# Optimization experiments

Hardware: AMD Instinct MI355X
Metric: run time of the kernel (lower is better)

Reference implementation:

```python
import jax, jax.numpy as jnp
import numpy as np

B, N, K, E, H, V = 128, 256, 4, 300, 150, 32000  # batch, nodes/tree, max children, embed, hidden, vocab
DELTA = 1.0


def setup_inputs() -> dict:
    key = jax.random.key(0)
    ks = jax.random.split(key, 8)
    query = jax.random.randint(ks[0], (B, N), 0, V, dtype=jnp.int32)
    pos = jax.random.randint(ks[1], (B, N), 0, V, dtype=jnp.int32)
    neg = jax.random.randint(ks[2], (B, N), 0, V, dtype=jnp.int32)
    # Complete K-ary tree over N nodes: children of node t are {K*t+1, ..., K*t+K} < N; root = node 0.
    ch = np.full((N, K), -1, dtype=np.int32)
    for t in range(N):
        for j in range(K):
            c = K * t + 1 + j
            if c < N:
                ch[t, j] = c
    children = jnp.asarray(ch)
    emb = jax.random.normal(ks[3], (V, E), dtype=jnp.float32) * 0.02
    W_iou = jax.random.normal(ks[4], (E, 3 * H), dtype=jnp.float32) * 0.05
    U_iou = jax.random.normal(ks[5], (H, 3 * H), dtype=jnp.float32) * 0.05
    b_iou = jnp.zeros((3 * H,), jnp.float32)
    W_f = jax.random.normal(ks[6], (E, H), dtype=jnp.float32) * 0.05
    U_f = jax.random.normal(ks[7], (H, H), dtype=jnp.float32) * 0.05
    b_f = jnp.zeros((H,), jnp.float32)
    return {"query": query, "pos": pos, "neg": neg, "children": children,
            "emb": emb, "W_iou": W_iou, "U_iou": U_iou, "b_iou": b_iou,
            "W_f": W_f, "U_f": U_f, "b_f": b_f}


def _childsum_treelstm(x, children, W_iou, U_iou, b_iou, W_f, U_f, b_f):
    """x: [B, N, E] node embeddings. Returns root (c, h): each [B, H]."""
    Bn, Nn, _ = x.shape
    Hh = U_f.shape[0]
    h0 = jnp.zeros((Bn, Nn, Hh), x.dtype)
    c0 = jnp.zeros((Bn, Nn, Hh), x.dtype)

    def step(carry, t):
        h_all, c_all = carry
        ch = children[t]                        # [K] child indices, -1 = padding
        mask = (ch >= 0)
        idx = jnp.where(mask, ch, 0)
        m = mask.astype(x.dtype)[None, :, None]  # [1, K, 1]
        h_k = h_all[:, idx] * m                 # [B, K, H]
        c_k = c_all[:, idx] * m
        h_sum = h_k.sum(axis=1)                 # child-sum h_tilde [B, H]
        x_t = x[:, t]                           # [B, E]
        iou = x_t @ W_iou + h_sum @ U_iou + b_iou
        i, o, u = jnp.split(iou, 3, axis=-1)
        i = jax.nn.sigmoid(i)
        o = jax.nn.sigmoid(o)
        u = jnp.tanh(u)
        # per-child forget gates: f_jk = sigmoid(W_f x_j + U_f h_k + b_f)
        f = jax.nn.sigmoid((x_t @ W_f + b_f)[:, None, :] + h_k @ U_f)  # [B, K, H]
        c_t = i * u + (f * c_k).sum(axis=1)     # c_k already masked
        h_t = o * jnp.tanh(c_t)
        return (h_all.at[:, t].set(h_t), c_all.at[:, t].set(c_t)), None

    # children have larger indices than parents -> process N-1 .. 0 (root last)
    (h_all, c_all), _ = jax.lax.scan(step, (h0, c0), jnp.arange(Nn - 1, -1, -1))
    return c_all[:, 0], h_all[:, 0]


def _cosine(a, b):
    num = (a * b).sum(-1)
    den = jnp.sqrt((a * a).sum(-1) * (b * b).sum(-1)) + 1e-8
    return num / den


def reference(query, pos, neg, children, emb, W_iou, U_iou, b_iou, W_f, U_f, b_f):
    qc, _ = _childsum_treelstm(emb[query], children, W_iou, U_iou, b_iou, W_f, U_f, b_f)
    pc, _ = _childsum_treelstm(emb[pos], children, W_iou, U_iou, b_iou, W_f, U_f, b_f)
    nc, _ = _childsum_treelstm(emb[neg], children, W_iou, U_iou, b_iou, W_f, U_f, b_f)
    a = _cosine(qc, pc)  # [B]
    b = _cosine(qc, nc)  # [B]
    return jax.nn.relu(DELTA - a + b)
```

## Files before the change

kernel.cpp:

```cpp
#include <hip/hip_runtime.h>
#include <hip/hip_bf16.h>

typedef short short8 __attribute__((ext_vector_type(8)));
typedef float floatx4 __attribute__((ext_vector_type(4)));
typedef unsigned short ushort;

#define Bb 128
#define Nn 256
#define Hh 150
#define HK 160
#define Vv 32000
#define NROW 384
#define PROJC 640
#define NINT 64
#define ZROW (Vv + NROW * NINT)

__device__ __forceinline__ float sigf(float x) { return 1.0f / (1.0f + __expf(-x)); }
__device__ __forceinline__ float tanhf_(float x) { return 1.0f - 2.0f / (__expf(2.0f * x) + 1.0f); }
__device__ __forceinline__ float bf2f(ushort s) { union { float f; unsigned u; } v; v.u = ((unsigned)s) << 16; return v.f; }
__device__ __forceinline__ ushort f2bf(float f) { __hip_bfloat16 h = __float2bfloat16(f); return *(ushort*)&h; }

__global__ __launch_bounds__(256) void k_prep(
    const float* __restrict__ W_iou, const float* __restrict__ W_f,
    const float* __restrict__ U_iou, const float* __restrict__ U_f,
    const float* __restrict__ b_iou, const float* __restrict__ b_f,
    short* __restrict__ Wt, short* __restrict__ Uti, short* __restrict__ Utf,
    float* __restrict__ biasw, ushort* __restrict__ h_u, float* __restrict__ c_u)
{
    int idx = blockIdx.x * 256 + threadIdx.x;
    const int nWt = PROJC * 320, nUi = 464 * 160, nUf = 160 * 160;
    if (idx < nWt) {
        int n = idx / 320, k = idx % 320;
        int seg = n / 160, cc = n % 160;
        float v = 0.f;
        if (k < 300 && cc < 150) {
            if (seg == 0)      v = W_iou[k * 450 + cc];
            else if (seg == 1) v = W_iou[k * 450 + 150 + cc];
            else if (seg == 2) v = W_iou[k * 450 + 300 + cc];
            else               v = W_f[k * 150 + cc];
        }
        Wt[idx] = (short)f2bf(v);
    } else if (idx < nWt + nUi) {
        int i2 = idx - nWt; int n = i2 / 160, k = i2 % 160;
        float v = (k < 150 && n < 450) ? U_iou[k * 450 + n] : 0.f;
        Uti[i2] = (short)f2bf(v);
    } else if (idx < nWt + nUi + nUf) {
        int i2 = idx - nWt - nUi; int n = i2 / 160, k = i2 % 160;
        float v = (k < 150) ? U_f[k * 150 + n] : 0.f;
        Utf[i2] = (short)f2bf(v);
    } else if (idx < nWt + nUi + nUf + PROJC) {
        int n = idx - nWt - nUi - nUf;
        int seg = n / 160, cc = n % 160;
        biasw[n] = (cc < 150) ? (seg < 3 ? b_iou[seg * 150 + cc] : b_f[cc]) : 0.f;
    } else if (idx < nWt + nUi + nUf + PROJC + HK) {
        int k = idx - (nWt + nUi + nUf + PROJC);
        h_u[(long)ZROW * HK + k] = 0;
        c_u[(long)ZROW * HK + k] = 0.f;
    }
}

__global__ __launch_bounds__(256) void k_vproj(
    const float* __restrict__ emb, const short* __restrict__ Wt,
    const float* __restrict__ biasw, ushort* __restrict__ proj,
    ushort* __restrict__ h_u, float* __restrict__ c_u)
{
    __shared__ __align__(16) short As[32 * 328];
    const int tid = threadIdx.x;
    const int v0 = blockIdx.x * 32;

    for (int i = tid; i < 32 * 80; i += 256) {
        int r = i / 80, q = i % 80, k0 = q * 4;
        short4 sv;
        if (k0 < 300) {
            float4 x = *(const float4*)(emb + (long)(v0 + r) * 300 + k0);
            sv.x = (short)f2bf(x.x); sv.y = (short)f2bf(x.y);
            sv.z = (short)f2bf(x.z); sv.w = (short)f2bf(x.w);
        } else sv = make_short4(0, 0, 0, 0);
        *(short4*)&As[r * 328 + k0] = sv;
    }
    __syncthreads();

    const int w = tid >> 6, lane = tid & 63;
    const int m = lane & 15, kq = (lane >> 4) * 8;

    short8 a0[10], a1[10];
    #pragma unroll
    for (int ks = 0; ks < 10; ks++) {
        a0[ks] = *(const short8*)&As[m * 328 + kq + ks * 32];
        a1[ks] = *(const short8*)&As[(16 + m) * 328 + kq + ks * 32];
    }

    for (int j = w; j < 10; j += 4) {
        int col = j * 16 + m;
        const short* bp = Wt + (long)col * 320 + kq;
        floatx4 acc[4][2];
        #pragma unroll
        for (int s = 0; s < 4; s++) { acc[s][0] = {0.f,0.f,0.f,0.f}; acc[s][1] = {0.f,0.f,0.f,0.f}; }
        #pragma unroll
        for (int ks = 0; ks < 10; ks++) {
            short8 b0 = *(const short8*)(bp + 0 * 160 * 320 + ks * 32);
            short8 b1 = *(const short8*)(bp + 1 * 160 * 320 + ks * 32);
            short8 b2 = *(const short8*)(bp + 2 * 160 * 320 + ks * 32);
            short8 b3 = *(const short8*)(bp + 3 * 160 * 320 + ks * 32);
            acc[0][0] = __builtin_amdgcn_mfma_f32_16x16x32_bf16(a0[ks], b0, acc[0][0], 0, 0, 0);
            acc[0][1] = __builtin_amdgcn_mfma_f32_16x16x32_bf16(a1[ks], b0, acc[0][1], 0, 0, 0);
            acc[1][0] = __builtin_amdgcn_mfma_f32_16x16x32_bf16(a0[ks], b1, acc[1][0], 0, 0, 0);
            acc[1][1] = __builtin_amdgcn_mfma_f32_16x16x32_bf16(a1[ks], b1, acc[1][1], 0, 0, 0);
            acc[2][0] = __builtin_amdgcn_mfma_f32_16x16x32_bf16(a0[ks], b2, acc[2][0], 0, 0, 0);
            acc[2][1] = __builtin_amdgcn_mfma_f32_16x16x32_bf16(a1[ks], b2, acc[2][1], 0, 0, 0);
            acc[3][0] = __builtin_amdgcn_mfma_f32_16x16x32_bf16(a0[ks], b3, acc[3][0], 0, 0, 0);
            acc[3][1] = __builtin_amdgcn_mfma_f32_16x16x32_bf16(a1[ks], b3, acc[3][1], 0, 0, 0);
        }

        float bi_ = biasw[col], bo_ = biasw[160 + col];
        float bu_ = biasw[320 + col], bf_ = biasw[480 + col];
        int rb = (lane >> 4) * 4;
        #pragma unroll
        for (int g = 0; g < 2; g++) {
            #pragma unroll
            for (int reg = 0; reg < 4; reg++) {
                long row = v0 + g * 16 + rb + reg;
                float pi = acc[0][g][reg] + bi_;
                float po = acc[1][g][reg] + bo_;
                float pu = acc[2][g][reg] + bu_;
                float pf = acc[3][g][reg] + bf_;
                ushort* pr = proj + row * PROJC;
                pr[col]       = f2bf(pi);
                pr[160 + col] = f2bf(po);
                pr[320 + col] = f2bf(pu);
                pr[480 + col] = f2bf(pf);
                float iv = sigf(pi), ov = sigf(po), uv = tanhf_(pu);
                float cc = iv * uv;
                c_u[row * HK + col] = cc;
                h_u[row * HK + col] = f2bf(ov * tanhf_(cc));
            }
        }
    }
}

__global__ __launch_bounds__(256) void k_level(
    int t0,
    const int* __restrict__ tq, const int* __restrict__ tp, const int* __restrict__ tn,
    const int* __restrict__ children, const ushort* __restrict__ proj,
    const short* __restrict__ Uti, const short* __restrict__ Utf,
    ushort* __restrict__ h_u, float* __restrict__ c_u)
{
    __shared__ __align__(16) short As[5][16][168];
    __shared__ int idx_s[16][4];
    __shared__ int tok_s[16];

    const int tid = threadIdx.x;
    const int t = t0 + blockIdx.x / 24;
    const int r0 = (blockIdx.x % 24) * 16;

    if (tid < 64) {
        int r = tid >> 2, j = tid & 3;
        int rg = r0 + r, g = rg >> 7, b = rg & 127;
        const int* tok = (g == 0) ? tq : (g == 1 ? tp : tn);
        int ch = children[t * 4 + j];
        int idx;
        if (ch < 0)        idx = ZROW;
        else if (ch >= 64) idx = tok[b * Nn + ch];
        else               idx = Vv + rg * NINT + ch;
        idx_s[r][j] = idx;
        if (j == 0) tok_s[r] = tok[b * Nn + t];
    }
    __syncthreads();

    for (int i = tid; i < 16 * 20; i += 256) {
        int r = i / 20, k0 = (i % 20) * 8;
        int4 v0 = *(const int4*)(h_u + (long)idx_s[r][0] * HK + k0);
        int4 v1 = *(const int4*)(h_u + (long)idx_s[r][1] * HK + k0);
        int4 v2 = *(const int4*)(h_u + (long)idx_s[r][2] * HK + k0);
        int4 v3 = *(const int4*)(h_u + (long)idx_s[r][3] * HK + k0);
        *(int4*)&As[1][r][k0] = v0;
        *(int4*)&As[2][r][k0] = v1;
        *(int4*)&As[3][r][k0] = v2;
        *(int4*)&As[4][r][k0] = v3;
        ushort s[8];
        const ushort* p0 = (const ushort*)&v0; const ushort* p1 = (const ushort*)&v1;
        const ushort* p2 = (const ushort*)&v2; const ushort* p3 = (const ushort*)&v3;
        #pragma unroll
        for (int e = 0; e < 8; e++)
            s[e] = f2bf(bf2f(p0[e]) + bf2f(p1[e]) + bf2f(p2[e]) + bf2f(p3[e]));
        *(int4*)&As[0][r][k0] = *(int4*)s;
    }
    __syncthreads();

    const int w = tid >> 6, lane = tid & 63;
    const int m = lane & 15, kq = (lane >> 4) * 8;
    const int rbase = (lane >> 4) * 4;

    for (int nt = w; nt < 10; nt += 4) {
        int col = nt * 16 + m;

        ushort pg[4][4]; float cg[4][4];
        #pragma unroll
        for (int reg = 0; reg < 4; reg++) {
            const ushort* pr = proj + (long)tok_s[rbase + reg] * PROJC;
            pg[0][reg] = pr[col];
            pg[1][reg] = pr[160 + col];
            pg[2][reg] = pr[320 + col];
            pg[3][reg] = pr[480 + col];
            #pragma unroll
            for (int j = 0; j < 4; j++)
                cg[j][reg] = c_u[(long)idx_s[rbase + reg][j] * HK + col];
        }

        const short* bi  = Uti + (long)(col) * HK + kq;
        const short* bo  = Uti + (long)(150 + col) * HK + kq;
        const short* bu  = Uti + (long)(300 + col) * HK + kq;
        const short* bff = Utf + (long)col * HK + kq;
        floatx4 ai = {0.f,0.f,0.f,0.f}, ao = ai, au = ai;
        floatx4 af0 = ai, af1 = ai, af2 = ai, af3 = ai;
        #pragma unroll
        for (int ks = 0; ks < 5; ks++) {
            short8 asum = *(const short8*)&As[0][m][kq + ks * 32];
            short8 ac0  = *(const short8*)&As[1][m][kq + ks * 32];
            short8 ac1  = *(const short8*)&As[2][m][kq + ks * 32];
            short8 ac2  = *(const short8*)&As[3][m][kq + ks * 32];
            short8 ac3  = *(const short8*)&As[4][m][kq + ks * 32];
            short8 vbi = *(const short8*)(bi + ks * 32);
            short8 vbo = *(const short8*)(bo + ks * 32);
            short8 vbu = *(const short8*)(bu + ks * 32);
            short8 vbf = *(const short8*)(bff + ks * 32);
            ai  = __builtin_amdgcn_mfma_f32_16x16x32_bf16(asum, vbi, ai, 0, 0, 0);
            ao  = __builtin_amdgcn_mfma_f32_16x16x32_bf16(asum, vbo, ao, 0, 0, 0);
            au  = __builtin_amdgcn_mfma_f32_16x16x32_bf16(asum, vbu, au, 0, 0, 0);
            af0 = __builtin_amdgcn_mfma_f32_16x16x32_bf16(ac0,  vbf, af0, 0, 0, 0);
            af1 = __builtin_amdgcn_mfma_f32_16x16x32_bf16(ac1,  vbf, af1, 0, 0, 0);
            af2 = __builtin_amdgcn_mfma_f32_16x16x32_bf16(ac2,  vbf, af2, 0, 0, 0);
            af3 = __builtin_amdgcn_mfma_f32_16x16x32_bf16(ac3,  vbf, af3, 0, 0, 0);
        }

        if (col < Hh) {
            #pragma unroll
            for (int reg = 0; reg < 4; reg++) {
                int rg = r0 + rbase + reg;
                float iv = sigf(bf2f(pg[0][reg])   + ai[reg]);
                float ov = sigf(bf2f(pg[1][reg])   + ao[reg]);
                float uv = tanhf_(bf2f(pg[2][reg]) + au[reg]);
                float fpre = bf2f(pg[3][reg]);
                float cv = iv * uv;
                cv = fmaf(sigf(fpre + af0[reg]), cg[0][reg], cv);
                cv = fmaf(sigf(fpre + af1[reg]), cg[1][reg], cv);
                cv = fmaf(sigf(fpre + af2[reg]), cg[2][reg], cv);
                cv = fmaf(sigf(fpre + af3[reg]), cg[3][reg], cv);
                long o = (long)(Vv + rg * NINT + t) * HK + col;
                c_u[o] = cv;
                h_u[o] = f2bf(ov * tanhf_(cv));
            }
        } else {
            #pragma unroll
            for (int reg = 0; reg < 4; reg++) {
                long o = (long)(Vv + (r0 + rbase + reg) * NINT + t) * HK + col;
                c_u[o] = 0.f; h_u[o] = 0;
            }
        }
    }
}

__global__ __launch_bounds__(64) void k_cos(const float* __restrict__ c_u, float* __restrict__ out)
{
    int b = blockIdx.x, tid = threadIdx.x;
    const float* qc = c_u + (long)(Vv + (0 * Bb + b) * NINT) * HK;
    const float* pc = c_u + (long)(Vv + (1 * Bb + b) * NINT) * HK;
    const float* nc = c_u + (long)(Vv + (2 * Bb + b) * NINT) * HK;
    float qp = 0, qn = 0, qq = 0, pp = 0, nn2 = 0;
    for (int k = tid; k < Hh; k += 64) {
        float qv = qc[k], pv = pc[k], nv = nc[k];
        qp += qv * pv; qn += qv * nv; qq += qv * qv; pp += pv * pv; nn2 += nv * nv;
    }
    #pragma unroll
    for (int off = 32; off > 0; off >>= 1) {
        qp += __shfl_down(qp, off, 64);
        qn += __shfl_down(qn, off, 64);
        qq += __shfl_down(qq, off, 64);
        pp += __shfl_down(pp, off, 64);
        nn2 += __shfl_down(nn2, off, 64);
    }
    if (tid == 0) {
        float a = qp / (sqrtf(qq * pp) + 1e-8f);
        float d = qn / (sqrtf(qq * nn2) + 1e-8f);
        out[b] = fmaxf(0.0f, 1.0f - a + d);
    }
}

extern "C" void kernel_launch(void* const* d_in, const int* in_sizes, int n_in,
                              void* d_out, int out_size, void* d_ws, size_t ws_size,
                              hipStream_t stream)
{
    const int*   tq       = (const int*)d_in[0];
    const int*   tp       = (const int*)d_in[1];
    const int*   tn       = (const int*)d_in[2];
    const int*   children = (const int*)d_in[3];
    const float* emb      = (const float*)d_in[4];
    const float* W_iou    = (const float*)d_in[5];
    const float* U_iou    = (const float*)d_in[6];
    const float* b_iou    = (const float*)d_in[7];
    const float* W_f      = (const float*)d_in[8];
    const float* U_f      = (const float*)d_in[9];
    const float* b_f      = (const float*)d_in[10];
    float* out = (float*)d_out;

    char* ws = (char*)d_ws;
    ushort* proj  = (ushort*)ws;
    ushort* h_u   = (ushort*)(ws + 40960000);
    float*  c_u   = (float*)(ws + 59064640);
    short*  Wt    = (short*)(ws + 95273920);
    short*  Uti   = (short*)(ws + 95683520);
    short*  Utf   = (short*)(ws + 95832000);
    float*  biasw = (float*)(ws + 95883200);

    k_prep<<<1194, 256, 0, stream>>>(W_iou, W_f, U_iou, U_f, b_iou, b_f,
                                     Wt, Uti, Utf, biasw, h_u, c_u);
    k_vproj<<<Vv / 32, 256, 0, stream>>>(emb, Wt, biasw, proj, h_u, c_u);
    k_level<<<43 * 24, 256, 0, stream>>>(21, tq, tp, tn, children, proj, Uti, Utf, h_u, c_u);
    k_level<<<16 * 24, 256, 0, stream>>>(5,  tq, tp, tn, children, proj, Uti, Utf, h_u, c_u);
    k_level<<<4 * 24, 256, 0, stream>>>(1,   tq, tp, tn, children, proj, Uti, Utf, h_u, c_u);
    k_level<<<1 * 24, 256, 0, stream>>>(0,   tq, tp, tn, children, proj, Uti, Utf, h_u, c_u);
    k_cos<<<Bb, 64, 0, stream>>>(c_u, out);
}
```

Before: 286.6 us.

## Store projection in MFMA-fragment layout, coalesce vproj stores, split small levels wider

k_vproj now writes the gate projections in a tiled layout matching the MFMA accumulator fragment, as packed 8-byte stores instead of scattered 2-byte stores. The h/c leaf states are staged through shared memory so they go out as 16-byte row-contiguous writes. k_level computes the matching fragment addresses to read proj, and its small upper levels spread the column tiles over more blocks (G parameter) to raise parallelism. The cost is more complex address arithmetic and gather loads deferred into the epilogue instead of being issued before the MFMA loop.

```diff
diff --git a/kernel.cpp b/kernel.cpp
--- a/kernel.cpp
+++ b/kernel.cpp
@@ -11,7 +11,6 @@
 #define HK 160
 #define Vv 32000
 #define NROW 384
-#define PROJC 640
 #define NINT 64
 #define ZROW (Vv + NROW * NINT)
 
@@ -28,7 +27,7 @@
     float* __restrict__ biasw, ushort* __restrict__ h_u, float* __restrict__ c_u)
 {
     int idx = blockIdx.x * 256 + threadIdx.x;
-    const int nWt = PROJC * 320, nUi = 464 * 160, nUf = 160 * 160;
+    const int nWt = 640 * 320, nUi = 464 * 160, nUf = 160 * 160;
     if (idx < nWt) {
         int n = idx / 320, k = idx % 320;
         int seg = n / 160, cc = n % 160;
@@ -48,12 +47,12 @@
         int i2 = idx - nWt - nUi; int n = i2 / 160, k = i2 % 160;
         float v = (k < 150) ? U_f[k * 150 + n] : 0.f;
         Utf[i2] = (short)f2bf(v);
-    } else if (idx < nWt + nUi + nUf + PROJC) {
+    } else if (idx < nWt + nUi + nUf + 640) {
         int n = idx - nWt - nUi - nUf;
         int seg = n / 160, cc = n % 160;
         biasw[n] = (cc < 150) ? (seg < 3 ? b_iou[seg * 150 + cc] : b_f[cc]) : 0.f;
-    } else if (idx < nWt + nUi + nUf + PROJC + HK) {
-        int k = idx - (nWt + nUi + nUf + PROJC);
+    } else if (idx < nWt + nUi + nUf + 640 + HK) {
+        int k = idx - (nWt + nUi + nUf + 640);
         h_u[(long)ZROW * HK + k] = 0;
         c_u[(long)ZROW * HK + k] = 0.f;
     }
@@ -65,6 +64,8 @@
     ushort* __restrict__ h_u, float* __restrict__ c_u)
 {
     __shared__ __align__(16) short As[32 * 328];
+    __shared__ __align__(16) float Tc[4][32][20];
+    __shared__ __align__(16) ushort Th[4][32][24];
     const int tid = threadIdx.x;
     const int v0 = blockIdx.x * 32;
 
@@ -81,7 +82,7 @@
     __syncthreads();
 
     const int w = tid >> 6, lane = tid & 63;
-    const int m = lane & 15, kq = (lane >> 4) * 8;
+    const int m = lane & 15, quad = lane >> 4, kq = quad * 8;
 
     short8 a0[10], a1[10];
     #pragma unroll
@@ -112,34 +113,55 @@
             acc[3][1] = __builtin_amdgcn_mfma_f32_16x16x32_bf16(a1[ks], b3, acc[3][1], 0, 0, 0);
         }
 
-        float bi_ = biasw[col], bo_ = biasw[160 + col];
-        float bu_ = biasw[320 + col], bf_ = biasw[480 + col];
-        int rb = (lane >> 4) * 4;
-        #pragma unroll
-        for (int g = 0; g < 2; g++) {
+        float bias[4] = { biasw[col], biasw[160 + col], biasw[320 + col], biasw[480 + col] };
+        float pre[4][2][4];
+        #pragma unroll
+        for (int s = 0; s < 4; s++)
+            #pragma unroll
+            for (int g = 0; g < 2; g++)
+                #pragma unroll
+                for (int reg = 0; reg < 4; reg++)
+                    pre[s][g][reg] = acc[s][g][reg] + bias[s];
+
+        long tbase = (long)(blockIdx.x * 10 + j) * 2048;
+        #pragma unroll
+        for (int s = 0; s < 4; s++)
+            #pragma unroll
+            for (int g = 0; g < 2; g++) {
+                unsigned u0 = (unsigned)f2bf(pre[s][g][0]) | ((unsigned)f2bf(pre[s][g][1]) << 16);
+                unsigned u1 = (unsigned)f2bf(pre[s][g][2]) | ((unsigned)f2bf(pre[s][g][3]) << 16);
+                *(uint2*)(proj + tbase + s * 512 + g * 256 + lane * 4) = make_uint2(u0, u1);
+            }
+
+        #pragma unroll
+        for (int g = 0; g < 2; g++)
             #pragma unroll
             for (int reg = 0; reg < 4; reg++) {
-                long row = v0 + g * 16 + rb + reg;
-                float pi = acc[0][g][reg] + bi_;
-                float po = acc[1][g][reg] + bo_;
-                float pu = acc[2][g][reg] + bu_;
-                float pf = acc[3][g][reg] + bf_;
-                ushort* pr = proj + row * PROJC;
-                pr[col]       = f2bf(pi);
-                pr[160 + col] = f2bf(po);
-                pr[320 + col] = f2bf(pu);
-                pr[480 + col] = f2bf(pf);
-                float iv = sigf(pi), ov = sigf(po), uv = tanhf_(pu);
+                float iv = sigf(pre[0][g][reg]);
+                float ov = sigf(pre[1][g][reg]);
+                float uv = tanhf_(pre[2][g][reg]);
                 float cc = iv * uv;
-                c_u[row * HK + col] = cc;
-                h_u[row * HK + col] = f2bf(ov * tanhf_(cc));
-            }
-        }
+                int rr = g * 16 + quad * 4 + reg;
+                Tc[w][rr][m] = cc;
+                Th[w][rr][m] = f2bf(ov * tanhf_(cc));
+            }
+        asm volatile("s_waitcnt lgkmcnt(0)" ::: "memory");
+        {
+            int row = lane >> 1, half = lane & 1;
+            int4 hv = *(const int4*)&Th[w][row][half * 8];
+            *(int4*)(h_u + (long)(v0 + row) * HK + j * 16 + half * 8) = hv;
+            #pragma unroll
+            for (int qq = half; qq < 4; qq += 2) {
+                float4 cv4 = *(const float4*)&Tc[w][row][qq * 4];
+                *(float4*)(c_u + (long)(v0 + row) * HK + j * 16 + qq * 4) = cv4;
+            }
+        }
+        asm volatile("s_waitcnt lgkmcnt(0)" ::: "memory");
     }
 }
 
 __global__ __launch_bounds__(256) void k_level(
-    int t0,
+    int t0, int G,
     const int* __restrict__ tq, const int* __restrict__ tp, const int* __restrict__ tn,
     const int* __restrict__ children, const ushort* __restrict__ proj,
     const short* __restrict__ Uti, const short* __restrict__ Utf,
@@ -150,8 +172,10 @@
     __shared__ int tok_s[16];
 
     const int tid = threadIdx.x;
-    const int t = t0 + blockIdx.x / 24;
-    const int r0 = (blockIdx.x % 24) * 16;
+    const int gi = blockIdx.x % G;
+    const int rest = blockIdx.x / G;
+    const int t = t0 + rest / 24;
+    const int r0 = (rest % 24) * 16;
 
     if (tid < 64) {
         int r = tid >> 2, j = tid & 3;
@@ -191,22 +215,8 @@
     const int m = lane & 15, kq = (lane >> 4) * 8;
     const int rbase = (lane >> 4) * 4;
 
-    for (int nt = w; nt < 10; nt += 4) {
+    for (int nt = gi * 4 + w; nt < 10; nt += 4 * G) {
         int col = nt * 16 + m;
-
-        ushort pg[4][4]; float cg[4][4];
-        #pragma unroll
-        for (int reg = 0; reg < 4; reg++) {
-            const ushort* pr = proj + (long)tok_s[rbase + reg] * PROJC;
-            pg[0][reg] = pr[col];
-            pg[1][reg] = pr[160 + col];
-            pg[2][reg] = pr[320 + col];
-            pg[3][reg] = pr[480 + col];
-            #pragma unroll
-            for (int j = 0; j < 4; j++)
-                cg[j][reg] = c_u[(long)idx_s[rbase + reg][j] * HK + col];
-        }
-
         const short* bi  = Uti + (long)(col) * HK + kq;
         const short* bo  = Uti + (long)(150 + col) * HK + kq;
         const short* bu  = Uti + (long)(300 + col) * HK + kq;
@@ -237,15 +247,19 @@
             #pragma unroll
             for (int reg = 0; reg < 4; reg++) {
                 int rg = r0 + rbase + reg;
-                float iv = sigf(bf2f(pg[0][reg])   + ai[reg]);
-                float ov = sigf(bf2f(pg[1][reg])   + ao[reg]);
-                float uv = tanhf_(bf2f(pg[2][reg]) + au[reg]);
-                float fpre = bf2f(pg[3][reg]);
+                int v = tok_s[rbase + reg];
+                int vb = v >> 5, rr = v & 31;
+                const ushort* pb = proj + ((long)(vb * 10 + nt)) * 2048
+                                 + (rr >> 4) * 256 + (((rr >> 2) & 3) * 16 + m) * 4 + (rr & 3);
+                float iv = sigf(bf2f(pb[0])      + ai[reg]);
+                float ov = sigf(bf2f(pb[512])    + ao[reg]);
+                float uv = tanhf_(bf2f(pb[1024]) + au[reg]);
+                float fpre = bf2f(pb[1536]);
                 float cv = iv * uv;
-                cv = fmaf(sigf(fpre + af0[reg]), cg[0][reg], cv);
-                cv = fmaf(sigf(fpre + af1[reg]), cg[1][reg], cv);
-                cv = fmaf(sigf(fpre + af2[reg]), cg[2][reg], cv);
-                cv = fmaf(sigf(fpre + af3[reg]), cg[3][reg], cv);
+                cv = fmaf(sigf(fpre + af0[reg]), c_u[(long)idx_s[rbase + reg][0] * HK + col], cv);
+                cv = fmaf(sigf(fpre + af1[reg]), c_u[(long)idx_s[rbase + reg][1] * HK + col], cv);
+                cv = fmaf(sigf(fpre + af2[reg]), c_u[(long)idx_s[rbase + reg][2] * HK + col], cv);
+                cv = fmaf(sigf(fpre + af3[reg]), c_u[(long)idx_s[rbase + reg][3] * HK + col], cv);
                 long o = (long)(Vv + rg * NINT + t) * HK + col;
                 c_u[o] = cv;
                 h_u[o] = f2bf(ov * tanhf_(cv));
@@ -315,9 +329,9 @@
     k_prep<<<1194, 256, 0, stream>>>(W_iou, W_f, U_iou, U_f, b_iou, b_f,
                                      Wt, Uti, Utf, biasw, h_u, c_u);
     k_vproj<<<Vv / 32, 256, 0, stream>>>(emb, Wt, biasw, proj, h_u, c_u);
-    k_level<<<43 * 24, 256, 0, stream>>>(21, tq, tp, tn, children, proj, Uti, Utf, h_u, c_u);
-    k_level<<<16 * 24, 256, 0, stream>>>(5,  tq, tp, tn, children, proj, Uti, Utf, h_u, c_u);
-    k_level<<<4 * 24, 256, 0, stream>>>(1,   tq, tp, tn, children, proj, Uti, Utf, h_u, c_u);
-    k_level<<<1 * 24, 256, 0, stream>>>(0,   tq, tp, tn, children, proj, Uti, Utf, h_u, c_u);
+    k_level<<<43 * 24 * 1, 256, 0, stream>>>(21, 1, tq, tp, tn, children, proj, Uti, Utf, h_u, c_u);
+    k_level<<<16 * 24 * 2, 256, 0, stream>>>(5,  2, tq, tp, tn, children, proj, Uti, Utf, h_u, c_u);
+    k_level<<<4 * 24 * 3, 256, 0, stream>>>(1,   3, tq, tp, tn, children, proj, Uti, Utf, h_u, c_u);
+    k_level<<<1 * 24 * 3, 256, 0, stream>>>(0,   3, tq, tp, tn, children, proj, Uti, Utf, h_u, c_u);
     k_cos<<<Bb, 64, 0, stream>>>(c_u, out);
 }
```

Result: slower. 292.8 us (+2.1%).
